# Kernel optimization log

Hardware: AMD Instinct MI355X
Metric: run time of the kernel (lower is better)

## Reference

```python
import jax, jax.numpy as jnp
import numpy as np

H = 8       # heads (cross and self)
L = 6       # self-attention layers per block
EPS = 1e-5  # torch LayerNorm eps


def layernorm(x, w, b):
    mu = jnp.mean(x, axis=-1, keepdims=True)
    var = jnp.mean((x - mu) ** 2, axis=-1, keepdims=True)
    return (x - mu) * jax.lax.rsqrt(var + EPS) * w + b


def mha(xq, xkv, wq, bq, wk, bk, wv, bv, wo, bo):
    # xq: [B,N,Dq], xkv: [B,M,Ckv]
    B, N, _ = xq.shape
    q = xq @ wq + bq
    k = xkv @ wk + bk
    v = xkv @ wv + bv
    split = lambda t: t.reshape(t.shape[0], t.shape[1], H, -1).transpose(0, 2, 1, 3)
    q, k, v = split(q), split(k), split(v)  # [B,H,n,c]
    scale = q.shape[-1] ** -0.5
    attn = jax.nn.softmax(jnp.einsum('bhic,bhjc->bhij', q, k) * scale, axis=-1)
    o = jnp.einsum('bhij,bhjc->bhic', attn, v)
    o = o.transpose(0, 2, 1, 3).reshape(B, N, -1)
    return o @ wo + bo


def mlp(x, lnw, lnb, w1, b1, w2, b2):
    h = layernorm(x, lnw, lnb)
    return jax.nn.gelu(h @ w1 + b1, approximate=False) @ w2 + b2


def setup_inputs() -> dict:
    key = jax.random.key(0)
    ks = jax.random.split(key, 16)
    B, M, C = 8, 4096, 512
    N, D, W = 512, 1024, 4
    s = 0.02
    w = lambda k, shape: jax.random.normal(k, shape, jnp.float32) * s
    return dict(
        x=jax.random.normal(ks[0], (B, M, C), jnp.float32),
        latent=w(ks[1], (N, D)),
        ca_qn_w=jnp.ones(D), ca_qn_b=jnp.zeros(D),
        ca_kvn_w=jnp.ones(C), ca_kvn_b=jnp.zeros(C),
        ca_wq=w(ks[2], (D, D)), ca_bq=jnp.zeros(D),
        ca_wk=w(ks[3], (C, D)), ca_bk=jnp.zeros(D),
        ca_wv=w(ks[4], (C, D)), ca_bv=jnp.zeros(D),
        ca_wo=w(ks[5], (D, D)), ca_bo=jnp.zeros(D),
        ca_ln_w=jnp.ones(D), ca_ln_b=jnp.zeros(D),
        ca_w1=w(ks[6], (D, W * D)), ca_b1=jnp.zeros(W * D),
        ca_w2=w(ks[7], (W * D, D)), ca_b2=jnp.zeros(D),
        sa_n_w=jnp.ones((L, D)), sa_n_b=jnp.zeros((L, D)),
        sa_wq=w(ks[8], (L, D, D)), sa_bq=jnp.zeros((L, D)),
        sa_wk=w(ks[9], (L, D, D)), sa_bk=jnp.zeros((L, D)),
        sa_wv=w(ks[10], (L, D, D)), sa_bv=jnp.zeros((L, D)),
        sa_wo=w(ks[11], (L, D, D)), sa_bo=jnp.zeros((L, D)),
        sa_ln_w=jnp.ones((L, D)), sa_ln_b=jnp.zeros((L, D)),
        sa_w1=w(ks[12], (L, D, W * D)), sa_b1=jnp.zeros((L, W * D)),
        sa_w2=w(ks[13], (L, W * D, D)), sa_b2=jnp.zeros((L, D)),
    )


def reference(x, latent, ca_qn_w, ca_qn_b, ca_kvn_w, ca_kvn_b,
              ca_wq, ca_bq, ca_wk, ca_bk, ca_wv, ca_bv, ca_wo, ca_bo,
              ca_ln_w, ca_ln_b, ca_w1, ca_b1, ca_w2, ca_b2,
              sa_n_w, sa_n_b, sa_wq, sa_bq, sa_wk, sa_bk, sa_wv, sa_bv,
              sa_wo, sa_bo, sa_ln_w, sa_ln_b, sa_w1, sa_b1, sa_w2, sa_b2):
    B = x.shape[0]
    lat = jnp.broadcast_to(latent, (B,) + latent.shape)  # [B,N,D]
    # cross-attention layer (pre-LN, residual) + MLP residual
    h = mha(layernorm(lat, ca_qn_w, ca_qn_b), layernorm(x, ca_kvn_w, ca_kvn_b),
            ca_wq, ca_bq, ca_wk, ca_bk, ca_wv, ca_bv, ca_wo, ca_bo) + lat
    h = mlp(h, ca_ln_w, ca_ln_b, ca_w1, ca_b1, ca_w2, ca_b2) + h
    # self-attention block (num_self_attention_blocks = 1)
    for i in range(L):
        hn = layernorm(h, sa_n_w[i], sa_n_b[i])
        a = mha(hn, hn, sa_wq[i], sa_bq[i], sa_wk[i], sa_bk[i],
                sa_wv[i], sa_bv[i], sa_wo[i], sa_bo[i]) + h
        h = mlp(a, sa_ln_w[i], sa_ln_b[i], sa_w1[i], sa_b1[i], sa_w2[i], sa_b2[i]) + a
    return h
```

## Files before the change

kernel.cpp:

```cpp
#include <hip/hip_runtime.h>


typedef short  short8  __attribute__((ext_vector_type(8)));
typedef unsigned short ushort8v __attribute__((ext_vector_type(8)));
typedef float  f32x4   __attribute__((ext_vector_type(4)));

__device__ __forceinline__ unsigned short f2bf(float f) {
  unsigned int u = __builtin_bit_cast(unsigned int, f);
  u += 0x7FFFu + ((u >> 16) & 1u);
  return (unsigned short)(u >> 16);
}

__device__ __forceinline__ void async16(const void* g, void* l) {
  __builtin_amdgcn_global_load_lds(
      (const __attribute__((address_space(1))) unsigned int*)g,
      (__attribute__((address_space(3))) unsigned int*)l, 16, 0, 0);
}

__device__ __forceinline__ f32x4 mfma_bf16(short8 a, short8 b, f32x4 c) {
  return __builtin_amdgcn_mfma_f32_16x16x32_bf16(a, b, c, 0, 0, 0);
}

template <int MODE>
__global__ __launch_bounds__(256)
void gemm_bt(const unsigned short* __restrict__ A,
             const unsigned short* __restrict__ Bt,
             const float* __restrict__ bias,
             const float* __restrict__ resid,
             void* __restrict__ Cp,
             int M, int N, int K)
{
  __shared__ unsigned short As[128 * 64];
  __shared__ unsigned short Bs[128 * 64];
  const int tid = (int)threadIdx.x;
  const int w = tid >> 6, l = tid & 63, g = l >> 4, p = l & 15;
  const int wr = w >> 1, wc = w & 1;
  const long brow = (long)blockIdx.y * 128;
  const long bcol = (long)blockIdx.x * 128;
  const int crow = l >> 3;
  const int ccol = (l & 7) * 8;

  f32x4 acc[4][4] = {};

  for (int k0 = 0; k0 < K; k0 += 64) {
    __syncthreads();
#pragma unroll
    for (int i = 0; i < 4; ++i) {
      const int ch = w * 4 + i;
      const long rA = brow + ch * 8 + crow;
      async16(A + rA * (long)K + k0 + ccol, (char*)As + ch * 1024);
      const long rB = bcol + ch * 8 + crow;
      async16(Bt + rB * (long)K + k0 + ccol, (char*)Bs + ch * 1024);
    }
    __syncthreads();
#pragma unroll
    for (int ks = 0; ks < 2; ++ks) {
      short8 af[4], bfr[4];
#pragma unroll
      for (int m = 0; m < 4; ++m) {
        const int row = wr * 64 + m * 16 + p;
        af[m] = *(const short8*)((const char*)As + row * 128 + ks * 64 + g * 16);
      }
#pragma unroll
      for (int n = 0; n < 4; ++n) {
        const int row = wc * 64 + n * 16 + p;
        bfr[n] = *(const short8*)((const char*)Bs + row * 128 + ks * 64 + g * 16);
      }
#pragma unroll
      for (int m = 0; m < 4; ++m)
#pragma unroll
        for (int n = 0; n < 4; ++n)
          acc[m][n] = mfma_bf16(af[m], bfr[n], acc[m][n]);
    }
  }

#pragma unroll
  for (int n = 0; n < 4; ++n) {
    const long col = bcol + wc * 64 + n * 16 + p;
    const float bv = bias[col];
#pragma unroll
    for (int m = 0; m < 4; ++m) {
      const long row0 = brow + wr * 64 + m * 16 + g * 4;
#pragma unroll
      for (int r = 0; r < 4; ++r) {
        float v = acc[m][n][r] + bv;
        const long off = (row0 + r) * (long)N + col;
        if constexpr (MODE == 1)
          v = 0.5f * v * (1.0f + erff(v * 0.70710678118654752f));
        if constexpr (MODE == 2)
          ((float*)Cp)[off] = v + resid[off];
        else
          ((unsigned short*)Cp)[off] = f2bf(v);
      }
    }
  }
}

__global__ __launch_bounds__(256)
void flash_attn(const unsigned short* __restrict__ Q,
                const unsigned short* __restrict__ Kp,
                const unsigned short* __restrict__ Vt,
                unsigned short* __restrict__ O,
                int Mk, long qBatchStride, float c1)
{
  __shared__ unsigned short Ks[64 * 128];
  __shared__ unsigned short Vs[128 * 64];
  const int tid = (int)threadIdx.x;
  const int w = tid >> 6, l = tid & 63, g = l >> 4, p = l & 15;
  const int b = (int)blockIdx.y >> 3, h = (int)blockIdx.y & 7;
  const int q0 = (int)blockIdx.x * 64 + w * 16;

  const unsigned short* qptr =
      Q + (long)b * qBatchStride + (long)(q0 + p) * 1024 + h * 128 + g * 8;
  short8 qf[4];
#pragma unroll
  for (int ks = 0; ks < 4; ++ks) qf[ks] = *(const short8*)(qptr + ks * 32);

  const unsigned short* Kb = Kp + (long)b * Mk * 1024 + h * 128;
  const unsigned short* Vb = Vt + ((long)b * 1024 + h * 128) * (long)Mk;

  f32x4 oacc[8] = {};
  float m_run = -3.0e38f, l_run = 0.0f;

  for (int kt = 0; kt < Mk; kt += 64) {
    __syncthreads();
#pragma unroll
    for (int i = 0; i < 4; ++i) {
      const int ch = w * 4 + i;
      {
        const int tr = ch * 4 + (l >> 4);
        const int cb = ((l & 15) * 16) ^ ((tr & 7) << 4);
        async16(Kb + (long)(kt + tr) * 1024 + (cb >> 1), (char*)Ks + ch * 1024);
      }
      {
        const int tr = ch * 8 + (l >> 3);
        const int cb = ((l & 7) * 16) ^ ((tr & 7) << 4);
        async16(Vb + (long)tr * Mk + kt + (cb >> 1), (char*)Vs + ch * 1024);
      }
    }
    __syncthreads();

    f32x4 sacc[4] = {};
#pragma unroll
    for (int ks = 0; ks < 4; ++ks)
#pragma unroll
      for (int s = 0; s < 4; ++s) {
        const int row = s * 16 + p;
        const int cb = (ks * 64 + g * 16) ^ ((row & 7) << 4);
        const short8 kf = *(const short8*)((const char*)Ks + row * 256 + cb);
        sacc[s] = mfma_bf16(kf, qf[ks], sacc[s]);
      }

    float mt = -3.0e38f;
#pragma unroll
    for (int s = 0; s < 4; ++s)
#pragma unroll
      for (int r = 0; r < 4; ++r) mt = fmaxf(mt, sacc[s][r]);
    mt = fmaxf(mt, __shfl_xor(mt, 16));
    mt = fmaxf(mt, __shfl_xor(mt, 32));
    const float m_new = fmaxf(m_run, mt);
    const float corr = exp2f((m_run - m_new) * c1);
    float P[4][4];
    float ls = 0.0f;
#pragma unroll
    for (int s = 0; s < 4; ++s)
#pragma unroll
      for (int r = 0; r < 4; ++r) {
        const float e = exp2f((sacc[s][r] - m_new) * c1);
        P[s][r] = e; ls += e;
      }
    ls += __shfl_xor(ls, 16);
    ls += __shfl_xor(ls, 32);
    l_run = l_run * corr + ls;
    m_run = m_new;
#pragma unroll
    for (int t = 0; t < 8; ++t)
#pragma unroll
      for (int r = 0; r < 4; ++r) oacc[t][r] *= corr;

    float pf[2][8];
#pragma unroll
    for (int s = 0; s < 4; ++s)
#pragma unroll
      for (int r = 0; r < 4; ++r)
#pragma unroll
        for (int hf = 0; hf < 2; ++hf) {
          const float tv = __shfl(P[s][r], ((g & 1) * 2 + hf) * 16 + p);
          if ((g >> 1) == (s & 1)) pf[s >> 1][(hf << 2) | r] = tv;
        }
    short8 pb[2];
#pragma unroll
    for (int ks2 = 0; ks2 < 2; ++ks2) {
      ushort8v t8;
#pragma unroll
      for (int jj = 0; jj < 8; ++jj) t8[jj] = f2bf(pf[ks2][jj]);
      pb[ks2] = __builtin_bit_cast(short8, t8);
    }

#pragma unroll
    for (int ks2 = 0; ks2 < 2; ++ks2)
#pragma unroll
      for (int t = 0; t < 8; ++t) {
        const int row = t * 16 + p;
        const int cb = (ks2 * 64 + g * 16) ^ ((row & 7) << 4);
        const short8 vf = *(const short8*)((const char*)Vs + row * 128 + cb);
        oacc[t] = mfma_bf16(vf, pb[ks2], oacc[t]);
      }
  }

  __syncthreads();
  const float inv = 1.0f / l_run;
  char* om = (char*)Ks + w * 4096;
#pragma unroll
  for (int t = 0; t < 8; ++t) {
    const int cbase = t * 32 + g * 8;
    const int off = p * 256 + (cbase ^ ((p & 7) << 4));
    uint2 pk;
    pk.x = (unsigned int)f2bf(oacc[t][0] * inv) |
           ((unsigned int)f2bf(oacc[t][1] * inv) << 16);
    pk.y = (unsigned int)f2bf(oacc[t][2] * inv) |
           ((unsigned int)f2bf(oacc[t][3] * inv) << 16);
    *(uint2*)(om + off) = pk;
  }
  const int q = l >> 2;
  const int chb0 = (l & 3) * 64;
  unsigned short* obase =
      O + ((long)b * 512 + q0 + q) * 1024 + h * 128 + (chb0 >> 1);
#pragma unroll
  for (int i = 0; i < 4; ++i) {
    const int off = q * 256 + ((chb0 + i * 16) ^ ((q & 7) << 4));
    const short8 vv = *(const short8*)(om + off);
    *(short8*)(obase + i * 8) = vv;
  }
}

__global__ __launch_bounds__(256)
void ln_kernel(const float* __restrict__ x, const float* __restrict__ gw,
               const float* __restrict__ gb, unsigned short* __restrict__ y,
               int cols)
{
  const long row = blockIdx.x;
  const float* xr = x + row * (long)cols;
  unsigned short* yr = y + row * (long)cols;
  float s = 0.0f, s2 = 0.0f;
  for (int c = (int)threadIdx.x * 4; c < cols; c += 1024) {
    const float4 v = *(const float4*)(xr + c);
    s  += v.x + v.y + v.z + v.w;
    s2 += v.x * v.x + v.y * v.y + v.z * v.z + v.w * v.w;
  }
#pragma unroll
  for (int o = 32; o; o >>= 1) { s += __shfl_xor(s, o); s2 += __shfl_xor(s2, o); }
  __shared__ float rs_[4], rs2_[4];
  const int wv = (int)threadIdx.x >> 6;
  if ((threadIdx.x & 63) == 0) { rs_[wv] = s; rs2_[wv] = s2; }
  __syncthreads();
  s  = rs_[0] + rs_[1] + rs_[2] + rs_[3];
  s2 = rs2_[0] + rs2_[1] + rs2_[2] + rs2_[3];
  const float invn = 1.0f / (float)cols;
  const float mu = s * invn;
  const float var = fmaxf(s2 * invn - mu * mu, 0.0f);
  const float rstd = rsqrtf(var + 1e-5f);
  for (int c = (int)threadIdx.x * 4; c < cols; c += 1024) {
    const float4 v = *(const float4*)(xr + c);
    const float4 w4 = *(const float4*)(gw + c);
    const float4 b4 = *(const float4*)(gb + c);
    ushort4 o;
    o.x = f2bf((v.x - mu) * rstd * w4.x + b4.x);
    o.y = f2bf((v.y - mu) * rstd * w4.y + b4.y);
    o.z = f2bf((v.z - mu) * rstd * w4.z + b4.z);
    o.w = f2bf((v.w - mu) * rstd * w4.w + b4.w);
    *(ushort4*)(yr + c) = o;
  }
}

__global__ __launch_bounds__(256)
void tw_kernel(const float* __restrict__ in, unsigned short* __restrict__ out,
               int R, int Cc)
{
  __shared__ float t[32][33];
  const int tx = (int)threadIdx.x & 31, ty = (int)threadIdx.x >> 5;
  const long c0 = (long)blockIdx.x * 32;
  const long r0 = (long)blockIdx.y * 32;
#pragma unroll
  for (int j = 0; j < 4; ++j)
    t[ty + j * 8][tx] = in[(r0 + ty + j * 8) * (long)Cc + c0 + tx];
  __syncthreads();
#pragma unroll
  for (int j = 0; j < 4; ++j)
    out[(c0 + ty + j * 8) * (long)R + r0 + tx] = f2bf(t[tx][ty + j * 8]);
}

__global__ __launch_bounds__(256)
void tb_kernel(const unsigned short* __restrict__ in,
               unsigned short* __restrict__ out, int R, int Cc)
{
  __shared__ unsigned short t[32][33];
  const long zoff = (long)blockIdx.z * (long)R * Cc;
  const int tx = (int)threadIdx.x & 31, ty = (int)threadIdx.x >> 5;
  const long c0 = (long)blockIdx.x * 32;
  const long r0 = (long)blockIdx.y * 32;
#pragma unroll
  for (int j = 0; j < 4; ++j)
    t[ty + j * 8][tx] = in[zoff + (r0 + ty + j * 8) * (long)Cc + c0 + tx];
  __syncthreads();
#pragma unroll
  for (int j = 0; j < 4; ++j)
    out[zoff + (c0 + ty + j * 8) * (long)R + r0 + tx] = t[tx][ty + j * 8];
}

__global__ __launch_bounds__(256)
void bcast_kernel(const float* __restrict__ in, float* __restrict__ out)
{
  const int i = (int)(blockIdx.x * 256 + threadIdx.x);
  ((float4*)out)[i] = ((const float4*)in)[i & 131071];
}

extern "C" void kernel_launch(void* const* d_in, const int* in_sizes, int n_in,
                              void* d_out, int out_size, void* d_ws,
                              size_t ws_size, hipStream_t stream)
{
  (void)in_sizes; (void)n_in; (void)out_size; (void)ws_size;
  const int Bx = 8, Mx = 4096, Cx = 512, Nx = 512, Dx = 1024, DDx = 4096, Lx = 6;
  const int TN = Bx * Nx;
  const int TM = Bx * Mx;
  const float c1 = 0.08838834764831845f * 1.44269504088896340f;

  const float* x      = (const float*)d_in[0];
  const float* latent = (const float*)d_in[1];
  const float* ca_qn_w = (const float*)d_in[2];
  const float* ca_qn_b = (const float*)d_in[3];
  const float* ca_kvn_w = (const float*)d_in[4];
  const float* ca_kvn_b = (const float*)d_in[5];
  const float* ca_wq = (const float*)d_in[6];
  const float* ca_bq = (const float*)d_in[7];
  const float* ca_wk = (const float*)d_in[8];
  const float* ca_bk = (const float*)d_in[9];
  const float* ca_wv = (const float*)d_in[10];
  const float* ca_bv = (const float*)d_in[11];
  const float* ca_wo = (const float*)d_in[12];
  const float* ca_bo = (const float*)d_in[13];
  const float* ca_ln_w = (const float*)d_in[14];
  const float* ca_ln_b = (const float*)d_in[15];
  const float* ca_w1 = (const float*)d_in[16];
  const float* ca_b1 = (const float*)d_in[17];
  const float* ca_w2 = (const float*)d_in[18];
  const float* ca_b2 = (const float*)d_in[19];
  const float* sa_n_w = (const float*)d_in[20];
  const float* sa_n_b = (const float*)d_in[21];
  const float* sa_wq = (const float*)d_in[22];
  const float* sa_bq = (const float*)d_in[23];
  const float* sa_wk = (const float*)d_in[24];
  const float* sa_bk = (const float*)d_in[25];
  const float* sa_wv = (const float*)d_in[26];
  const float* sa_bv = (const float*)d_in[27];
  const float* sa_wo = (const float*)d_in[28];
  const float* sa_bo = (const float*)d_in[29];
  const float* sa_ln_w = (const float*)d_in[30];
  const float* sa_ln_b = (const float*)d_in[31];
  const float* sa_w1 = (const float*)d_in[32];
  const float* sa_b1 = (const float*)d_in[33];
  const float* sa_w2 = (const float*)d_in[34];
  const float* sa_b2 = (const float*)d_in[35];

  char* wp = (char*)d_ws;
  auto alloc = [&](size_t bytes) {
    char* r = wp; wp += (bytes + 255) & ~(size_t)255; return r;
  };
  float* hA = (float*)alloc((size_t)TN * Dx * 4);
  float* hB = (float*)alloc((size_t)TN * Dx * 4);
  unsigned short* lnb  = (unsigned short*)alloc((size_t)TN * Dx * 2);
  unsigned short* qb   = (unsigned short*)alloc((size_t)TN * Dx * 2);
  unsigned short* ob   = (unsigned short*)alloc((size_t)TN * Dx * 2);
  unsigned short* mlpb = (unsigned short*)alloc((size_t)TN * DDx * 2);
  unsigned short* Kb   = (unsigned short*)alloc((size_t)TM * Dx * 2);
  unsigned short* Vb   = (unsigned short*)alloc((size_t)TM * Dx * 2);
  unsigned short* VTb  = (unsigned short*)alloc((size_t)TM * Dx * 2);
  unsigned short* wtq  = (unsigned short*)alloc((size_t)Dx * Dx * 2);
  unsigned short* wtk  = (unsigned short*)alloc((size_t)Dx * Dx * 2);
  unsigned short* wtv  = (unsigned short*)alloc((size_t)Dx * Dx * 2);
  unsigned short* wto  = (unsigned short*)alloc((size_t)Dx * Dx * 2);
  unsigned short* wtm1 = (unsigned short*)alloc((size_t)Dx * DDx * 2);
  unsigned short* wtm2 = (unsigned short*)alloc((size_t)Dx * DDx * 2);

  const dim3 blk(256);
  auto TW = [&](const float* win, unsigned short* wout, int R, int Cc) {
    tw_kernel<<<dim3(Cc / 32, R / 32), blk, 0, stream>>>(win, wout, R, Cc);
  };
  auto LN = [&](const float* xin, const float* gw, const float* gb,
                unsigned short* y, int rows, int cols) {
    ln_kernel<<<dim3(rows), blk, 0, stream>>>(xin, gw, gb, y, cols);
  };
  auto G0 = [&](const unsigned short* A, const unsigned short* Bt2,
                const float* bias, unsigned short* out, int M2, int N2, int K2) {
    gemm_bt<0><<<dim3(N2 / 128, M2 / 128), blk, 0, stream>>>(
        A, Bt2, bias, nullptr, out, M2, N2, K2);
  };
  auto G1 = [&](const unsigned short* A, const unsigned short* Bt2,
                const float* bias, unsigned short* out, int M2, int N2, int K2) {
    gemm_bt<1><<<dim3(N2 / 128, M2 / 128), blk, 0, stream>>>(
        A, Bt2, bias, nullptr, out, M2, N2, K2);
  };
  auto G2 = [&](const unsigned short* A, const unsigned short* Bt2,
                const float* bias, const float* resid, float* out,
                int M2, int N2, int K2) {
    gemm_bt<2><<<dim3(N2 / 128, M2 / 128), blk, 0, stream>>>(
        A, Bt2, bias, resid, out, M2, N2, K2);
  };

  bcast_kernel<<<dim3(TN * Dx / 4 / 256), blk, 0, stream>>>(latent, hA);
  LN(latent, ca_qn_w, ca_qn_b, lnb, Nx, Dx);
  TW(ca_wq, wtq, Dx, Dx);
  G0(lnb, wtq, ca_bq, qb, Nx, Dx, Dx);
  LN(x, ca_kvn_w, ca_kvn_b, mlpb, TM, Cx);
  TW(ca_wk, wtk, Cx, Dx);
  G0(mlpb, wtk, ca_bk, Kb, TM, Dx, Cx);
  TW(ca_wv, wtv, Cx, Dx);
  G0(mlpb, wtv, ca_bv, Vb, TM, Dx, Cx);
  tb_kernel<<<dim3(Dx / 32, Mx / 32, Bx), blk, 0, stream>>>(Vb, VTb, Mx, Dx);
  flash_attn<<<dim3(Nx / 64, Bx * 8), blk, 0, stream>>>(
      qb, Kb, VTb, ob, Mx, 0L, c1);
  TW(ca_wo, wto, Dx, Dx);
  G2(ob, wto, ca_bo, hA, hB, TN, Dx, Dx);
  LN(hB, ca_ln_w, ca_ln_b, lnb, TN, Dx);
  TW(ca_w1, wtm1, Dx, DDx);
  G1(lnb, wtm1, ca_b1, mlpb, TN, DDx, Dx);
  TW(ca_w2, wtm2, DDx, Dx);
  G2(mlpb, wtm2, ca_b2, hB, hA, TN, Dx, DDx);

  for (int i = 0; i < Lx; ++i) {
    LN(hA, sa_n_w + (size_t)i * Dx, sa_n_b + (size_t)i * Dx, lnb, TN, Dx);
    TW(sa_wq + (size_t)i * Dx * Dx, wtq, Dx, Dx);
    G0(lnb, wtq, sa_bq + (size_t)i * Dx, qb, TN, Dx, Dx);
    TW(sa_wk + (size_t)i * Dx * Dx, wtk, Dx, Dx);
    G0(lnb, wtk, sa_bk + (size_t)i * Dx, Kb, TN, Dx, Dx);
    TW(sa_wv + (size_t)i * Dx * Dx, wtv, Dx, Dx);
    G0(lnb, wtv, sa_bv + (size_t)i * Dx, Vb, TN, Dx, Dx);
    tb_kernel<<<dim3(Dx / 32, Nx / 32, Bx), blk, 0, stream>>>(Vb, VTb, Nx, Dx);
    flash_attn<<<dim3(Nx / 64, Bx * 8), blk, 0, stream>>>(
        qb, Kb, VTb, ob, Nx, (long)Nx * Dx, c1);
    TW(sa_wo + (size_t)i * Dx * Dx, wto, Dx, Dx);
    G2(ob, wto, sa_bo + (size_t)i * Dx, hA, hB, TN, Dx, Dx);
    LN(hB, sa_ln_w + (size_t)i * Dx, sa_ln_b + (size_t)i * Dx, lnb, TN, Dx);
    TW(sa_w1 + (size_t)i * Dx * DDx, wtm1, Dx, DDx);
    G1(lnb, wtm1, sa_b1 + (size_t)i * DDx, mlpb, TN, DDx, Dx);
    TW(sa_w2 + (size_t)i * DDx * Dx, wtm2, DDx, Dx);
    float* outp = (i == Lx - 1) ? (float*)d_out : hA;
    G2(mlpb, wtm2, sa_b2 + (size_t)i * Dx, hB, outp, TN, Dx, DDx);
  }
}
```

Before: 2.876 ms.

## Replace GEMM with 256x256-tile double-buffered pipelined MFMA kernel

Replaces the 128x128 single-buffered GEMM with a 256x256-tile, 512-thread kernel. It uses a 128KB double-buffered LDS ring, swizzled async global-to-LDS loads, and interleaved barrier-separated MFMA phases with s_setprio. The goal is to raise per-block data reuse and overlap global loads with compute. The cost is a large cut in block count: the self-attention GEMMs over 4096 rows with N=1024 launch only 64 blocks. That can leave most CUs idle, and only one block fits per CU given the LDS footprint.

```diff
diff --git a/kernel.cpp b/kernel.cpp
--- a/kernel.cpp
+++ b/kernel.cpp
@@ -22,65 +22,104 @@
 }
 
 template <int MODE>
-__global__ __launch_bounds__(256)
-void gemm_bt(const unsigned short* __restrict__ A,
+__global__ __launch_bounds__(512, 2)
+void gemm256(const unsigned short* __restrict__ A,
              const unsigned short* __restrict__ Bt,
              const float* __restrict__ bias,
              const float* __restrict__ resid,
              void* __restrict__ Cp,
              int M, int N, int K)
 {
-  __shared__ unsigned short As[128 * 64];
-  __shared__ unsigned short Bs[128 * 64];
+  __shared__ __align__(1024) char lds[131072];
+  constexpr int A0 = 0, A1 = 32768, B0 = 65536, B1 = 98304;
+
   const int tid = (int)threadIdx.x;
-  const int w = tid >> 6, l = tid & 63, g = l >> 4, p = l & 15;
-  const int wr = w >> 1, wc = w & 1;
-  const long brow = (long)blockIdx.y * 128;
-  const long bcol = (long)blockIdx.x * 128;
-  const int crow = l >> 3;
-  const int ccol = (l & 7) * 8;
-
-  f32x4 acc[4][4] = {};
-
-  for (int k0 = 0; k0 < K; k0 += 64) {
-    __syncthreads();
-#pragma unroll
-    for (int i = 0; i < 4; ++i) {
-      const int ch = w * 4 + i;
-      const long rA = brow + ch * 8 + crow;
-      async16(A + rA * (long)K + k0 + ccol, (char*)As + ch * 1024);
-      const long rB = bcol + ch * 8 + crow;
-      async16(Bt + rB * (long)K + k0 + ccol, (char*)Bs + ch * 1024);
-    }
-    __syncthreads();
-#pragma unroll
-    for (int ks = 0; ks < 2; ++ks) {
-      short8 af[4], bfr[4];
-#pragma unroll
-      for (int m = 0; m < 4; ++m) {
-        const int row = wr * 64 + m * 16 + p;
-        af[m] = *(const short8*)((const char*)As + row * 128 + ks * 64 + g * 16);
-      }
-#pragma unroll
-      for (int n = 0; n < 4; ++n) {
-        const int row = wc * 64 + n * 16 + p;
-        bfr[n] = *(const short8*)((const char*)Bs + row * 128 + ks * 64 + g * 16);
-      }
-#pragma unroll
-      for (int m = 0; m < 4; ++m)
-#pragma unroll
-        for (int n = 0; n < 4; ++n)
-          acc[m][n] = mfma_bf16(af[m], bfr[n], acc[m][n]);
-    }
-  }
+  const int wv = tid >> 6, l = tid & 63, g = l >> 4, p = l & 15;
+  const int wr = wv >> 2, wc = wv & 3;
+  const long brow = (long)blockIdx.y * 256;
+  const long bcol = (long)blockIdx.x * 256;
+
+  const int srow   = l >> 2;
+  const int schunk = ((l & 3) ^ ((l >> 5) << 1)) * 8;
+  const unsigned short* Agl = A  + (brow + wv * 32 + srow) * (long)K + schunk;
+  const unsigned short* Bgl = Bt + (bcol + wv * 32 + srow) * (long)K + schunk;
+  const int slds = (wv * 4) * 1024;
+
+  const int rdsw = p * 64 + ((g ^ ((p >> 3) << 1)) << 4);
+
+  f32x4 acc[8][4] = {};
+  short8 af[8], bq[2];
+
+  auto SGA = [&](int bufoff, long kt, int hk) {
+    async16(Agl + kt + hk * 32,              lds + bufoff + slds + hk * 1024);
+    async16(Agl + 16 * (long)K + kt + hk * 32,
+            lds + bufoff + slds + (2 + hk) * 1024);
+  };
+  auto SGB = [&](int bufoff, long kt, int hk) {
+    async16(Bgl + kt + hk * 32,              lds + bufoff + slds + hk * 1024);
+    async16(Bgl + 16 * (long)K + kt + hk * 32,
+            lds + bufoff + slds + (2 + hk) * 1024);
+  };
+  auto LDA = [&](int bufoff, int ks) {
+#pragma unroll
+    for (int m = 0; m < 8; ++m)
+      af[m] = *(const short8*)(lds + bufoff +
+                               ((wr * 8 + m) * 2 + ks) * 1024 + rdsw);
+  };
+  auto LDB = [&](int bufoff, int nh, int ks) {
+#pragma unroll
+    for (int nn = 0; nn < 2; ++nn)
+      bq[nn] = *(const short8*)(lds + bufoff +
+                                ((wc * 4 + nh * 2 + nn) * 2 + ks) * 1024 + rdsw);
+  };
+  auto MF = [&](int nh) {
+    __builtin_amdgcn_s_setprio(1);
+#pragma unroll
+    for (int m = 0; m < 8; ++m)
+#pragma unroll
+      for (int nn = 0; nn < 2; ++nn)
+        acc[m][nh * 2 + nn] = mfma_bf16(af[m], bq[nn], acc[m][nh * 2 + nn]);
+    __builtin_amdgcn_s_setprio(0);
+  };
+#define VMW  asm volatile("s_waitcnt vmcnt(4)" ::: "memory")
+#define BAR  __builtin_amdgcn_s_barrier()
+
+  SGA(A0, 0, 0); SGB(B0, 0, 0); SGA(A0, 0, 1); SGB(B0, 0, 1);
+  VMW;
+  BAR;
+
+  const int niter = K >> 7;
+  for (int i = 0; i < niter; ++i) {
+    const long kc1 = (long)i * 128 + 64;
+    const long kn0 = (i + 1 < niter) ? (long)i * 128 + 128 : 0;
+
+    LDA(A0, 0); LDB(B0, 0, 0); SGA(A1, kc1, 0);
+    BAR; MF(0); BAR;
+    LDB(B0, 1, 0); SGB(B1, kc1, 0); VMW;
+    BAR; MF(1); BAR;
+    LDA(A0, 1); LDB(B0, 0, 1); SGA(A1, kc1, 1);
+    BAR; MF(0); BAR;
+    LDB(B0, 1, 1); SGB(B1, kc1, 1); VMW;
+    BAR; MF(1); BAR;
+    LDA(A1, 0); LDB(B1, 0, 0); SGA(A0, kn0, 0);
+    BAR; MF(0); BAR;
+    LDB(B1, 1, 0); SGB(B0, kn0, 0); VMW;
+    BAR; MF(1); BAR;
+    LDA(A1, 1); LDB(B1, 0, 1); SGA(A0, kn0, 1);
+    BAR; MF(0); BAR;
+    LDB(B1, 1, 1); SGB(B0, kn0, 1); VMW;
+    BAR; MF(1); BAR;
+  }
+#undef VMW
+#undef BAR
 
 #pragma unroll
   for (int n = 0; n < 4; ++n) {
     const long col = bcol + wc * 64 + n * 16 + p;
     const float bv = bias[col];
 #pragma unroll
-    for (int m = 0; m < 4; ++m) {
-      const long row0 = brow + wr * 64 + m * 16 + g * 4;
+    for (int m = 0; m < 8; ++m) {
+      const long row0 = brow + wr * 128 + m * 16 + g * 4;
 #pragma unroll
       for (int r = 0; r < 4; ++r) {
         float v = acc[m][n][r] + bv;
@@ -382,7 +421,7 @@
   unsigned short* wtm1 = (unsigned short*)alloc((size_t)Dx * DDx * 2);
   unsigned short* wtm2 = (unsigned short*)alloc((size_t)Dx * DDx * 2);
 
-  const dim3 blk(256);
+  const dim3 blk(256), gblk(512);
   auto TW = [&](const float* win, unsigned short* wout, int R, int Cc) {
     tw_kernel<<<dim3(Cc / 32, R / 32), blk, 0, stream>>>(win, wout, R, Cc);
   };
@@ -392,18 +431,18 @@
   };
   auto G0 = [&](const unsigned short* A, const unsigned short* Bt2,
                 const float* bias, unsigned short* out, int M2, int N2, int K2) {
-    gemm_bt<0><<<dim3(N2 / 128, M2 / 128), blk, 0, stream>>>(
+    gemm256<0><<<dim3(N2 / 256, M2 / 256), gblk, 0, stream>>>(
         A, Bt2, bias, nullptr, out, M2, N2, K2);
   };
   auto G1 = [&](const unsigned short* A, const unsigned short* Bt2,
                 const float* bias, unsigned short* out, int M2, int N2, int K2) {
-    gemm_bt<1><<<dim3(N2 / 128, M2 / 128), blk, 0, stream>>>(
+    gemm256<1><<<dim3(N2 / 256, M2 / 256), gblk, 0, stream>>>(
         A, Bt2, bias, nullptr, out, M2, N2, K2);
   };
   auto G2 = [&](const unsigned short* A, const unsigned short* Bt2,
                 const float* bias, const float* resid, float* out,
                 int M2, int N2, int K2) {
-    gemm_bt<2><<<dim3(N2 / 128, M2 / 128), blk, 0, stream>>>(
+    gemm256<2><<<dim3(N2 / 256, M2 / 256), gblk, 0, stream>>>(
         A, Bt2, bias, resid, out, M2, N2, K2);
   };
 
```

Result: slower. 2.958 ms (+2.8%).
